# Optimization experiments

Hardware: AMD Instinct MI355X
Metric: run time of the kernel (lower is better)

The kernel has to match this reference:

```python
import jax, jax.numpy as jnp
import numpy as np

B, S, H = 2, 2048, 2048           # batch, seq_len, hidden_size
NH, HD = 16, 128                  # num_heads, head_dim
ROPE_THETA = 10000.0


def _rope_cos_sin(seq_len, head_dim, dtype):
    # standard rotary embedding tables: [seq, head_dim]
    inv_freq = 1.0 / (ROPE_THETA ** (jnp.arange(0, head_dim, 2, dtype=jnp.float32) / head_dim))
    t = jnp.arange(seq_len, dtype=jnp.float32)
    freqs = jnp.einsum('s,d->sd', t, inv_freq)          # [S, HD/2]
    emb = jnp.concatenate([freqs, freqs], axis=-1)      # [S, HD]
    return jnp.cos(emb).astype(dtype), jnp.sin(emb).astype(dtype)


def _rotate_half(x):
    x1, x2 = jnp.split(x, 2, axis=-1)
    return jnp.concatenate([-x2, x1], axis=-1)


def _apply_rope(x, cos, sin):
    # x: [B, S, NH, HD]; cos/sin: [S, HD]
    return x * cos[None, :, None, :] + _rotate_half(x) * sin[None, :, None, :]


def setup_inputs() -> dict:
    key = jax.random.key(0)
    ks = jax.random.split(key, 10)
    hidden_states = jax.random.normal(ks[0], (B, S, H), dtype=jnp.float32)
    # causal mask: 1.0 where attention is disallowed (k > q), matching mask * -1e9 usage
    mask = jnp.triu(jnp.ones((S, S), dtype=jnp.float32), k=1)[None, None, :, :]
    mask = jnp.broadcast_to(mask, (B, 1, S, S))
    xav = 1.0 / np.sqrt(H)
    Wq = jax.random.uniform(ks[1], (H, NH, HD), jnp.float32, -xav, xav)
    Wk = jax.random.uniform(ks[2], (H, NH, HD), jnp.float32, -xav, xav)
    Wv = jax.random.uniform(ks[3], (H, NH, HD), jnp.float32, -xav, xav)
    Wo = jax.random.uniform(ks[4], (NH, HD, H), jnp.float32, -xav, xav)
    bq = jnp.zeros((NH, HD), jnp.float32)
    bk = jnp.zeros((NH, HD), jnp.float32)
    bv = jnp.zeros((NH, HD), jnp.float32)
    bo = jnp.zeros((H,), jnp.float32)
    return {"hidden_states": hidden_states, "mask": mask, "Wq": Wq, "bq": bq,
            "Wk": Wk, "bk": bk, "Wv": Wv, "bv": bv, "Wo": Wo, "bo": bo}


def reference(hidden_states, mask, Wq, bq, Wk, bk, Wv, bv, Wo, bo):
    dtype = hidden_states.dtype
    scale = 1.0 / jnp.sqrt(jnp.asarray(HD, dtype))
    # q/k/v projections: DenseGeneral hidden -> (heads, head_dim)
    q = jnp.einsum('bsh,bhd->bsnd'.replace('bhd', 'hnd'), hidden_states, Wq) + bq  # [B,S,NH,HD]
    k = jnp.einsum('bsh,hnd->bsnd', hidden_states, Wk) + bk
    v = jnp.einsum('bsh,hnd->bsnd', hidden_states, Wv) + bv
    cos, sin = _rope_cos_sin(hidden_states.shape[1], HD, dtype)
    q = _apply_rope(q, cos, sin)
    k = _apply_rope(k, cos, sin)
    # [B,NH,S,HD]
    q, k, v = (x.transpose(0, 2, 1, 3) for x in (q, k, v))
    attn_scores = jnp.einsum('bhqd,bhkd->bhqk', q, k) * scale
    attn_scores = attn_scores + mask * (-1e9)           # mask broadcasts over heads
    probs = jax.nn.softmax(attn_scores, axis=-1)
    attn_output = jnp.einsum('bhqk,bhkd->bhqd', probs, v)
    attn_output = attn_output.transpose(0, 2, 1, 3)      # [B,S,NH,HD]
    return jnp.einsum('bsnd,ndh->bsh', attn_output, Wo) + bo
```

## Files before the change

### kernel.cpp

```cpp
#include <hip/hip_runtime.h>
#include <hip/hip_bf16.h>

#define B_ 2
#define S_ 2048
#define H_ 2048
#define NH_ 16
#define HD_ 128
#define M_ (B_*S_)

typedef unsigned short u16;
typedef unsigned int u32;
typedef __attribute__((ext_vector_type(8))) short bhalf8_t;
typedef __attribute__((ext_vector_type(4))) float fx4_t;

__device__ __forceinline__ float bf2f(u16 v) {
    unsigned u = ((unsigned)v) << 16;
    return __builtin_bit_cast(float, u);
}
__device__ __forceinline__ u16 f2bf(float f) {
    unsigned u = __builtin_bit_cast(unsigned, f);
    unsigned r = u + 0x7fffu + ((u >> 16) & 1u);
    return (u16)(r >> 16);
}
__device__ __forceinline__ u16 f2bf_trunc(float f) {
    return (u16)(__builtin_bit_cast(unsigned, f) >> 16);
}
__device__ __forceinline__ void gload_lds16(const u16* g, u16* l) {
    __builtin_amdgcn_global_load_lds(
        (const __attribute__((address_space(1))) u32*)g,
        (__attribute__((address_space(3))) u32*)l, 16, 0, 0);
}

__global__ __launch_bounds__(256) void cvt_bf16_k(const float* __restrict__ in,
                                                  u16* __restrict__ out) {
    int i = blockIdx.x * 256 + threadIdx.x;
    float4 v = ((const float4*)in)[i];
    ushort4 o;
    o.x = f2bf(v.x); o.y = f2bf(v.y); o.z = f2bf(v.z); o.w = f2bf(v.w);
    ((ushort4*)out)[i] = o;
}

__global__ __launch_bounds__(256) void transpose_cvt4_k(const float* __restrict__ s0,
                                                        const float* __restrict__ s1,
                                                        const float* __restrict__ s2,
                                                        const float* __restrict__ s3,
                                                        u16* __restrict__ out) {
    const float* in = blockIdx.z == 0 ? s0 : blockIdx.z == 1 ? s1
                    : blockIdx.z == 2 ? s2 : s3;
    u16* dst = out + (size_t)blockIdx.z * H_ * H_;
    __shared__ u16 tile[64][65];
    int k0 = blockIdx.y * 64, n0 = blockIdx.x * 64;
    int t = threadIdx.x;
    for (int i = 0; i < 16; i++) {
        int idx = t + i * 256;
        int r = idx >> 6, c = idx & 63;
        tile[r][c] = f2bf(in[(size_t)(k0 + r) * H_ + n0 + c]);
    }
    __syncthreads();
    for (int i = 0; i < 16; i++) {
        int idx = t + i * 256;
        int r = idx >> 6, c = idx & 63;
        dst[(size_t)(n0 + r) * H_ + k0 + c] = tile[c][r];
    }
}

__global__ __launch_bounds__(256) void gemm_qkv(const u16* __restrict__ A,
                                                const u16* __restrict__ Bt,
                                                const float* __restrict__ bq,
                                                const float* __restrict__ bk,
                                                const float* __restrict__ bv,
                                                u16* __restrict__ qh,
                                                u16* __restrict__ kh,
                                                u16* __restrict__ vT) {
    const int Ksz = H_;
    __shared__ u16 As[128 * 64];
    __shared__ u16 Bs[128 * 64];
    int t = threadIdx.x;
    int wave = t >> 6, lane = t & 63;
    int lr = lane & 15, lq = lane >> 4;
    int m0 = blockIdx.y * 128, n0 = blockIdx.x * 128;
    int wm = (wave >> 1) * 64, wn = (wave & 1) * 64;

    fx4_t acc[4][4];
    for (int i = 0; i < 4; i++)
        for (int j = 0; j < 4; j++)
            acc[i][j] = (fx4_t){0.f, 0.f, 0.f, 0.f};

    for (int k0 = 0; k0 < Ksz; k0 += 64) {
        for (int i = 0; i < 4; i++) {
            int c = t + i * 256;
            int r = c >> 3, g = (c & 7) ^ (r & 7);
            gload_lds16(&A[(size_t)(m0 + r) * Ksz + k0 + g * 8], As + (size_t)c * 8);
            gload_lds16(&Bt[(size_t)(n0 + r) * Ksz + k0 + g * 8], Bs + (size_t)c * 8);
        }
        __syncthreads();
        for (int ds = 0; ds < 2; ds++) {
            bhalf8_t a[4], b[4];
            int cs = (ds * 4 + lq) ^ (lr & 7);
            for (int i = 0; i < 4; i++)
                a[i] = *(const bhalf8_t*)&As[(((wm + i * 16 + lr) << 3) + cs) * 8];
            for (int j = 0; j < 4; j++)
                b[j] = *(const bhalf8_t*)&Bs[(((wn + j * 16 + lr) << 3) + cs) * 8];
            for (int i = 0; i < 4; i++)
                for (int j = 0; j < 4; j++)
                    acc[i][j] = __builtin_amdgcn_mfma_f32_16x16x32_bf16(a[i], b[j], acc[i][j], 0, 0, 0);
        }
        __syncthreads();
    }
    int which = n0 >> 11;
    const float* bias = which == 0 ? bq : which == 1 ? bk : bv;
    for (int i = 0; i < 4; i++)
        for (int j = 0; j < 4; j++) {
            int row0 = m0 + wm + i * 16 + lq * 4;
            int cc = (n0 & 2047) + wn + j * 16 + lr;
            float bvv = bias[cc];
            int bb = row0 >> 11, s = row0 & 2047;
            int hh = cc >> 7, d = cc & 127;
            if (which == 2) {
                ushort4 w;
                w.x = f2bf(acc[i][j][0] + bvv);
                w.y = f2bf(acc[i][j][1] + bvv);
                w.z = f2bf(acc[i][j][2] + bvv);
                w.w = f2bf(acc[i][j][3] + bvv);
                *(ushort4*)&vT[(((size_t)bb * NH_ + hh) * HD_ + d) * S_ + s] = w;
            } else {
                u16* dst = (which == 0 ? qh : kh);
                for (int r = 0; r < 4; r++)
                    dst[(((size_t)bb * NH_ + hh) * S_ + s + r) * HD_ + d] =
                        f2bf(acc[i][j][r] + bvv);
            }
        }
}

__global__ __launch_bounds__(256) void gemm_out(const u16* __restrict__ A,
                                                const u16* __restrict__ Bt,
                                                const float* __restrict__ bias,
                                                float* __restrict__ C) {
    const int Ksz = H_, Nsz = H_;
    __shared__ u16 As[128 * 64];
    __shared__ u16 Bs[128 * 64];
    int t = threadIdx.x;
    int wave = t >> 6, lane = t & 63;
    int lr = lane & 15, lq = lane >> 4;
    int m0 = blockIdx.y * 128, n0 = blockIdx.x * 128;
    int wm = (wave >> 1) * 64, wn = (wave & 1) * 64;

    fx4_t acc[4][4];
    for (int i = 0; i < 4; i++)
        for (int j = 0; j < 4; j++)
            acc[i][j] = (fx4_t){0.f, 0.f, 0.f, 0.f};

    for (int k0 = 0; k0 < Ksz; k0 += 64) {
        for (int i = 0; i < 4; i++) {
            int c = t + i * 256;
            int r = c >> 3, g = (c & 7) ^ (r & 7);
            gload_lds16(&A[(size_t)(m0 + r) * Ksz + k0 + g * 8], As + (size_t)c * 8);
            gload_lds16(&Bt[(size_t)(n0 + r) * Ksz + k0 + g * 8], Bs + (size_t)c * 8);
        }
        __syncthreads();
        for (int ds = 0; ds < 2; ds++) {
            bhalf8_t a[4], b[4];
            int cs = (ds * 4 + lq) ^ (lr & 7);
            for (int i = 0; i < 4; i++)
                a[i] = *(const bhalf8_t*)&As[(((wm + i * 16 + lr) << 3) + cs) * 8];
            for (int j = 0; j < 4; j++)
                b[j] = *(const bhalf8_t*)&Bs[(((wn + j * 16 + lr) << 3) + cs) * 8];
            for (int i = 0; i < 4; i++)
                for (int j = 0; j < 4; j++)
                    acc[i][j] = __builtin_amdgcn_mfma_f32_16x16x32_bf16(a[i], b[j], acc[i][j], 0, 0, 0);
        }
        __syncthreads();
    }
    for (int i = 0; i < 4; i++)
        for (int j = 0; j < 4; j++) {
            int row0 = m0 + wm + i * 16 + lq * 4;
            int col = n0 + wn + j * 16 + lr;
            float bvv = bias[col];
            for (int r = 0; r < 4; r++)
                C[(size_t)(row0 + r) * Nsz + col] = acc[i][j][r] + bvv;
        }
}

__global__ __launch_bounds__(256) void rope_k(u16* __restrict__ q, u16* __restrict__ k) {
    const float scale2 = 0.08838834764831845f * 1.44269504f;
    int idx = blockIdx.x * 256 + threadIdx.x;
    int i = idx & 63;
    int s = (idx >> 6) & 2047;
    int h = (idx >> 17) & 15;
    int b = idx >> 21;
    float inv = exp2f((float)i * (-13.287712379549449f / 64.0f));
    float ang = (float)s * inv;
    float sn, c;
    sincosf(ang, &sn, &c);
    size_t base = (((size_t)b * NH_ + h) * S_ + s) * HD_ + i;
    {
        float x1 = bf2f(q[base]), x2 = bf2f(q[base + 64]);
        q[base]      = f2bf((x1 * c - x2 * sn) * scale2);
        q[base + 64] = f2bf((x2 * c + x1 * sn) * scale2);
    }
    {
        float x1 = bf2f(k[base]), x2 = bf2f(k[base + 64]);
        k[base]      = f2bf(x1 * c - x2 * sn);
        k[base + 64] = f2bf(x2 * c + x1 * sn);
    }
}

#define PROW2 40
__global__ __launch_bounds__(256, 2) void flash_k(const u16* __restrict__ qh,
                                                  const u16* __restrict__ kh,
                                                  const u16* __restrict__ vT,
                                                  u16* __restrict__ attn) {
    __shared__ u16 sm[2 * 8192 + 2 * 8192 + 4 * 32 * PROW2];
    u16* KsB = sm;
    u16* VsB = sm + 16384;
    u16* Ps  = sm + 32768;

    int t = threadIdx.x, wave = t >> 6, lane = t & 63;
    int lr = lane & 15, lq = lane >> 4;
    int h = blockIdx.y, b = blockIdx.z;
    int ti = (b == 0) ? ((int)gridDim.x - 1 - (int)blockIdx.x) : (int)blockIdx.x;
    int q0 = ti * 128;

    const u16* kbase = kh + ((size_t)b * NH_ + h) * S_ * HD_;
    const u16* vbase = vT + ((size_t)b * NH_ + h) * HD_ * S_;
    u16* Pw = Ps + wave * 32 * PROW2;

    bhalf8_t aq[2][4];
#pragma unroll
    for (int rg = 0; rg < 2; rg++) {
        const u16* qrow =
            qh + (((size_t)b * NH_ + h) * S_ + q0 + wave * 32 + rg * 16 + lr) * HD_;
#pragma unroll
        for (int ds = 0; ds < 4; ds++)
            aq[rg][ds] = *(const bhalf8_t*)&qrow[ds * 32 + lq * 8];
    }

    float m_i[2][4], l_i[2][4];
    fx4_t acc_o[2][8];
#pragma unroll
    for (int rg = 0; rg < 2; rg++)
        for (int r = 0; r < 4; r++) { m_i[rg][r] = -INFINITY; l_i[rg][r] = 0.f; }
#pragma unroll
    for (int rg = 0; rg < 2; rg++)
        for (int dt = 0; dt < 8; dt++) acc_o[rg][dt] = (fx4_t){0.f, 0.f, 0.f, 0.f};

    bhalf8_t bones;
#pragma unroll
    for (int j = 0; j < 8; j++) bones[j] = (short)0x3F80;

    auto stageK = [&](int buf, int k0) {
        u16* dst = KsB + buf * 8192;
#pragma unroll
        for (int i = 0; i < 4; i++) {
            int c = t + i * 256;
            int r = c >> 4, g = (c & 15) ^ (r & 15);
            gload_lds16(&kbase[(size_t)(k0 + r) * HD_ + g * 8], dst + (size_t)c * 8);
        }
    };
    auto stageV = [&](int buf, int k0) {
        u16* dst = VsB + buf * 8192;
#pragma unroll
        for (int i = 0; i < 4; i++) {
            int c = t + i * 256;
            int r = c >> 3, g = (c & 7) ^ (r & 7);
            gload_lds16(&vbase[(size_t)r * S_ + k0 + g * 8], dst + (size_t)c * 8);
        }
    };

    int nkb = q0 / 64 + 2;
    stageK(0, 0);
    stageV(0, 0);
    for (int kbi = 0; kbi < nkb; kbi++) {
        int cur = kbi & 1;
        int k0 = kbi * 64;
        __syncthreads();
        if (kbi + 1 < nkb) {
            stageK(cur ^ 1, k0 + 64);
            stageV(cur ^ 1, k0 + 64);
        }
        const u16* Kc = KsB + cur * 8192;
        const u16* Vc = VsB + cur * 8192;

        bool active = (k0 <= q0 + wave * 32 + 31);

        fx4_t sacc[2][4];
        float alpha[2][4];
        if (active) {
#pragma unroll
            for (int rg = 0; rg < 2; rg++)
                for (int nt = 0; nt < 4; nt++)
                    sacc[rg][nt] = (fx4_t){0.f, 0.f, 0.f, 0.f};
            __builtin_amdgcn_s_setprio(1);
#pragma unroll
            for (int nt = 0; nt < 4; nt++) {
                int r = nt * 16 + lr;
#pragma unroll
                for (int ds = 0; ds < 4; ds++) {
                    bhalf8_t bk = *(const bhalf8_t*)&Kc[((r << 4) + ((ds * 4 + lq) ^ lr)) * 8];
                    sacc[0][nt] = __builtin_amdgcn_mfma_f32_16x16x32_bf16(aq[0][ds], bk, sacc[0][nt], 0, 0, 0);
                    sacc[1][nt] = __builtin_amdgcn_mfma_f32_16x16x32_bf16(aq[1][ds], bk, sacc[1][nt], 0, 0, 0);
                }
            }
            __builtin_amdgcn_s_setprio(0);

            if (kbi >= nkb - 2) {
#pragma unroll
                for (int rg = 0; rg < 2; rg++)
                    for (int nt = 0; nt < 4; nt++)
                        for (int r = 0; r < 4; r++) {
                            int kpos = k0 + nt * 16 + lr;
                            int qpos = q0 + wave * 32 + rg * 16 + lq * 4 + r;
                            if (kpos > qpos) sacc[rg][nt][r] = -1e30f;
                        }
            }

#pragma unroll
            for (int rg = 0; rg < 2; rg++) {
                float rmax[4];
#pragma unroll
                for (int r = 0; r < 4; r++)
                    rmax[r] = fmaxf(fmaxf(sacc[rg][0][r], sacc[rg][1][r]),
                                    fmaxf(sacc[rg][2][r], sacc[rg][3][r]));
#pragma unroll
                for (int off = 1; off < 16; off <<= 1)
                    for (int r = 0; r < 4; r++)
                        rmax[r] = fmaxf(rmax[r], __shfl_xor(rmax[r], off, 64));
#pragma unroll
                for (int r = 0; r < 4; r++) {
                    float mn = fmaxf(m_i[rg][r], rmax[r]);
                    alpha[rg][r] = exp2f(m_i[rg][r] - mn);
                    m_i[rg][r] = mn;
#pragma unroll
                    for (int nt = 0; nt < 4; nt++)
                        sacc[rg][nt][r] = exp2f(sacc[rg][nt][r] - mn);
                    l_i[rg][r] *= alpha[rg][r];
                }
#pragma unroll
                for (int dt = 0; dt < 8; dt++)
                    for (int r = 0; r < 4; r++) acc_o[rg][dt][r] *= alpha[rg][r];
            }

            fx4_t ls[2];
            ls[0] = (fx4_t){0.f, 0.f, 0.f, 0.f};
            ls[1] = (fx4_t){0.f, 0.f, 0.f, 0.f};
#pragma unroll
            for (int p = 0; p < 2; p++) {
#pragma unroll
                for (int rg = 0; rg < 2; rg++)
                    for (int nt2 = 0; nt2 < 2; nt2++)
                        for (int r = 0; r < 4; r++)
                            Pw[(rg * 16 + lq * 4 + r) * PROW2 + nt2 * 16 + lr] =
                                f2bf_trunc(sacc[rg][p * 2 + nt2][r]);
                __asm__ volatile("s_waitcnt lgkmcnt(0)" ::: "memory");
                bhalf8_t ap0 = *(const bhalf8_t*)&Pw[lr * PROW2 + lq * 8];
                bhalf8_t ap1 = *(const bhalf8_t*)&Pw[(16 + lr) * PROW2 + lq * 8];
                __builtin_amdgcn_s_setprio(1);
#pragma unroll
                for (int dt = 0; dt < 8; dt++) {
                    int r = dt * 16 + lr;
                    bhalf8_t bv = *(const bhalf8_t*)&Vc[((r << 3) + ((p * 4 + lq) ^ (lr & 7))) * 8];
                    acc_o[0][dt] = __builtin_amdgcn_mfma_f32_16x16x32_bf16(ap0, bv, acc_o[0][dt], 0, 0, 0);
                    acc_o[1][dt] = __builtin_amdgcn_mfma_f32_16x16x32_bf16(ap1, bv, acc_o[1][dt], 0, 0, 0);
                }
                ls[0] = __builtin_amdgcn_mfma_f32_16x16x32_bf16(ap0, bones, ls[0], 0, 0, 0);
                ls[1] = __builtin_amdgcn_mfma_f32_16x16x32_bf16(ap1, bones, ls[1], 0, 0, 0);
                __builtin_amdgcn_s_setprio(0);
            }
#pragma unroll
            for (int rg = 0; rg < 2; rg++)
                for (int r = 0; r < 4; r++) l_i[rg][r] += ls[rg][r];
        }
    }

#pragma unroll
    for (int rg = 0; rg < 2; rg++) {
        float rl[4];
#pragma unroll
        for (int r = 0; r < 4; r++) rl[r] = 1.f / l_i[rg][r];
#pragma unroll
        for (int dt = 0; dt < 8; dt++)
            for (int r = 0; r < 4; r++) {
                size_t row = (size_t)(b * S_ + q0 + wave * 32 + rg * 16 + lq * 4 + r);
                attn[(row * NH_ + h) * HD_ + dt * 16 + lr] = f2bf(acc_o[rg][dt][r] * rl[r]);
            }
    }
}

extern "C" void kernel_launch(void* const* d_in, const int* in_sizes, int n_in,
                              void* d_out, int out_size, void* d_ws, size_t ws_size,
                              hipStream_t stream) {
    const float* hs = (const float*)d_in[0];
    const float* Wq = (const float*)d_in[2];
    const float* bq = (const float*)d_in[3];
    const float* Wk = (const float*)d_in[4];
    const float* bk = (const float*)d_in[5];
    const float* Wv = (const float*)d_in[6];
    const float* bv = (const float*)d_in[7];
    const float* Wo = (const float*)d_in[8];
    const float* bo = (const float*)d_in[9];
    float* out = (float*)d_out;

    u16* ws   = (u16*)d_ws;
    size_t WW = (size_t)H_ * H_;
    size_t AC = (size_t)M_ * H_;
    u16* hsb  = ws;
    u16* Wall = hsb + AC;
    u16* WoT  = Wall + 3 * WW;
    u16* qh   = WoT + WW;
    u16* kh   = qh + AC;
    u16* vT   = kh + AC;
    u16* attn = vT + AC;

    dim3 tb(256);

    cvt_bf16_k<<<dim3(AC / (256 * 4)), tb, 0, stream>>>(hs, hsb);

    transpose_cvt4_k<<<dim3(32, 32, 4), tb, 0, stream>>>(Wq, Wk, Wv, Wo, Wall);

    gemm_qkv<<<dim3(3 * H_ / 128, M_ / 128), tb, 0, stream>>>(hsb, Wall, bq, bk, bv,
                                                              qh, kh, vT);

    rope_k<<<dim3((B_ * NH_ * S_ * 64) / 256), tb, 0, stream>>>(qh, kh);

    flash_k<<<dim3(S_ / 128, NH_, B_), tb, 0, stream>>>(qh, kh, vT, attn);

    gemm_out<<<dim3(H_ / 128, M_ / 128), tb, 0, stream>>>(attn, WoT, bo, out);
}
```

Baseline: 437.1 us.

## Rewrite QKV GEMM as 256x256 double-buffered 8-wave kernel with overlapped loads

```diff
diff --git a/kernel.cpp b/kernel.cpp
--- a/kernel.cpp
+++ b/kernel.cpp
@@ -30,6 +30,9 @@
         (const __attribute__((address_space(1))) u32*)g,
         (__attribute__((address_space(3))) u32*)l, 16, 0, 0);
 }
+#define ASM_BAR()   __asm__ volatile("s_barrier" ::: "memory")
+#define WAIT_VM0()  __asm__ volatile("s_waitcnt vmcnt(0)" ::: "memory")
+#define WAIT_LGKM0() __asm__ volatile("s_waitcnt lgkmcnt(0)" ::: "memory")
 
 __global__ __launch_bounds__(256) void cvt_bf16_k(const float* __restrict__ in,
                                                   u16* __restrict__ out) {
@@ -64,70 +67,121 @@
     }
 }
 
-__global__ __launch_bounds__(256) void gemm_qkv(const u16* __restrict__ A,
-                                                const u16* __restrict__ Bt,
-                                                const float* __restrict__ bq,
-                                                const float* __restrict__ bk,
-                                                const float* __restrict__ bv,
-                                                u16* __restrict__ qh,
-                                                u16* __restrict__ kh,
-                                                u16* __restrict__ vT) {
+__global__ __launch_bounds__(512, 2) void gemm_qkv8(const u16* __restrict__ A,
+                                                    const u16* __restrict__ Bt,
+                                                    const float* __restrict__ bq,
+                                                    const float* __restrict__ bk,
+                                                    const float* __restrict__ bv,
+                                                    u16* __restrict__ qh,
+                                                    u16* __restrict__ kh,
+                                                    u16* __restrict__ vT) {
     const int Ksz = H_;
-    __shared__ u16 As[128 * 64];
-    __shared__ u16 Bs[128 * 64];
+    __shared__ u16 sm8[4 * 16384];
     int t = threadIdx.x;
     int wave = t >> 6, lane = t & 63;
     int lr = lane & 15, lq = lane >> 4;
-    int m0 = blockIdx.y * 128, n0 = blockIdx.x * 128;
-    int wm = (wave >> 1) * 64, wn = (wave & 1) * 64;
-
-    fx4_t acc[4][4];
-    for (int i = 0; i < 4; i++)
+    int m0 = blockIdx.y * 256, n0 = blockIdx.x * 256;
+    int wm = (wave >> 2) * 128, wn = (wave & 3) * 64;
+
+    fx4_t acc[8][4];
+#pragma unroll
+    for (int i = 0; i < 8; i++)
         for (int j = 0; j < 4; j++)
             acc[i][j] = (fx4_t){0.f, 0.f, 0.f, 0.f};
 
-    for (int k0 = 0; k0 < Ksz; k0 += 64) {
+    auto stageA = [&](int buf, int k0) {
+        u16* dst = sm8 + buf * 16384;
+#pragma unroll
         for (int i = 0; i < 4; i++) {
-            int c = t + i * 256;
+            int c = t + i * 512;
             int r = c >> 3, g = (c & 7) ^ (r & 7);
-            gload_lds16(&A[(size_t)(m0 + r) * Ksz + k0 + g * 8], As + (size_t)c * 8);
-            gload_lds16(&Bt[(size_t)(n0 + r) * Ksz + k0 + g * 8], Bs + (size_t)c * 8);
-        }
-        __syncthreads();
-        for (int ds = 0; ds < 2; ds++) {
-            bhalf8_t a[4], b[4];
-            int cs = (ds * 4 + lq) ^ (lr & 7);
-            for (int i = 0; i < 4; i++)
-                a[i] = *(const bhalf8_t*)&As[(((wm + i * 16 + lr) << 3) + cs) * 8];
-            for (int j = 0; j < 4; j++)
-                b[j] = *(const bhalf8_t*)&Bs[(((wn + j * 16 + lr) << 3) + cs) * 8];
-            for (int i = 0; i < 4; i++)
-                for (int j = 0; j < 4; j++)
-                    acc[i][j] = __builtin_amdgcn_mfma_f32_16x16x32_bf16(a[i], b[j], acc[i][j], 0, 0, 0);
-        }
-        __syncthreads();
-    }
+            gload_lds16(&A[(size_t)(m0 + r) * Ksz + k0 + g * 8], dst + (size_t)c * 8);
+        }
+    };
+    auto stageB = [&](int buf, int k0) {
+        u16* dst = sm8 + 32768 + buf * 16384;
+#pragma unroll
+        for (int i = 0; i < 4; i++) {
+            int c = t + i * 512;
+            int r = c >> 3, g = (c & 7) ^ (r & 7);
+            gload_lds16(&Bt[(size_t)(n0 + r) * Ksz + k0 + g * 8], dst + (size_t)c * 8);
+        }
+    };
+
+    const int NT = Ksz / 64;
+    stageA(0, 0);
+    stageB(0, 0);
+    WAIT_VM0();
+    ASM_BAR();
+
+    for (int kt = 0; kt < NT; kt++) {
+        int cur = kt & 1;
+        const u16* Ab = sm8 + cur * 16384;
+        const u16* Bb = sm8 + 32768 + cur * 16384;
+        bhalf8_t bfr[8];
+
+#pragma unroll
+        for (int p = 0; p < 4; p++) {
+            if (p == 0) {
+#pragma unroll
+                for (int nj = 0; nj < 4; nj++)
+                    for (int ks = 0; ks < 2; ks++) {
+                        int row = wn + nj * 16 + lr;
+                        bfr[nj * 2 + ks] = *(const bhalf8_t*)
+                            &Bb[(((size_t)row << 3) + ((ks * 4 + lq) ^ (lr & 7))) * 8];
+                    }
+            }
+            bhalf8_t afr[2][2];
+#pragma unroll
+            for (int mi2 = 0; mi2 < 2; mi2++)
+                for (int ks = 0; ks < 2; ks++) {
+                    int row = wm + (p * 2 + mi2) * 16 + lr;
+                    afr[mi2][ks] = *(const bhalf8_t*)
+                        &Ab[(((size_t)row << 3) + ((ks * 4 + lq) ^ (lr & 7))) * 8];
+                }
+            if (kt + 1 < NT) {
+                if (p == 0) stageA(cur ^ 1, (kt + 1) * 64);
+                else if (p == 1) stageB(cur ^ 1, (kt + 1) * 64);
+            }
+            if (p == 3) WAIT_VM0();
+            ASM_BAR();
+            WAIT_LGKM0();
+            __builtin_amdgcn_sched_barrier(0);
+            __builtin_amdgcn_s_setprio(1);
+#pragma unroll
+            for (int mi2 = 0; mi2 < 2; mi2++)
+                for (int nj = 0; nj < 4; nj++)
+                    for (int ks = 0; ks < 2; ks++)
+                        acc[p * 2 + mi2][nj] = __builtin_amdgcn_mfma_f32_16x16x32_bf16(
+                            afr[mi2][ks], bfr[nj * 2 + ks], acc[p * 2 + mi2][nj], 0, 0, 0);
+            __builtin_amdgcn_s_setprio(0);
+            ASM_BAR();
+        }
+    }
+
     int which = n0 >> 11;
     const float* bias = which == 0 ? bq : which == 1 ? bk : bv;
-    for (int i = 0; i < 4; i++)
-        for (int j = 0; j < 4; j++) {
-            int row0 = m0 + wm + i * 16 + lq * 4;
-            int cc = (n0 & 2047) + wn + j * 16 + lr;
+#pragma unroll
+    for (int mi = 0; mi < 8; mi++)
+#pragma unroll
+        for (int nj = 0; nj < 4; nj++) {
+            int row0 = m0 + wm + mi * 16 + lq * 4;
+            int cc = (n0 & 2047) + wn + nj * 16 + lr;
             float bvv = bias[cc];
             int bb = row0 >> 11, s = row0 & 2047;
             int hh = cc >> 7, d = cc & 127;
             if (which == 2) {
                 ushort4 w;
-                w.x = f2bf(acc[i][j][0] + bvv);
-                w.y = f2bf(acc[i][j][1] + bvv);
-                w.z = f2bf(acc[i][j][2] + bvv);
-                w.w = f2bf(acc[i][j][3] + bvv);
+                w.x = f2bf(acc[mi][nj][0] + bvv);
+                w.y = f2bf(acc[mi][nj][1] + bvv);
+                w.z = f2bf(acc[mi][nj][2] + bvv);
+                w.w = f2bf(acc[mi][nj][3] + bvv);
                 *(ushort4*)&vT[(((size_t)bb * NH_ + hh) * HD_ + d) * S_ + s] = w;
             } else {
                 u16* dst = (which == 0 ? qh : kh);
                 for (int r = 0; r < 4; r++)
                     dst[(((size_t)bb * NH_ + hh) * S_ + s + r) * HD_ + d] =
-                        f2bf(acc[i][j][r] + bvv);
+                        f2bf(acc[mi][nj][r] + bvv);
             }
         }
 }
@@ -417,8 +471,9 @@
 
     transpose_cvt4_k<<<dim3(32, 32, 4), tb, 0, stream>>>(Wq, Wk, Wv, Wo, Wall);
 
-    gemm_qkv<<<dim3(3 * H_ / 128, M_ / 128), tb, 0, stream>>>(hsb, Wall, bq, bk, bv,
-                                                              qh, kh, vT);
+    gemm_qkv8<<<dim3(3 * H_ / 256, M_ / 256), dim3(512), 0, stream>>>(hsb, Wall,
+                                                                      bq, bk, bv,
+                                                                      qh, kh, vT);
 
     rope_k<<<dim3((B_ * NH_ * S_ * 64) / 256), tb, 0, stream>>>(qh, kh);
 
```

Measured after the change: 435.0 us. No clear change (-0.5%).
